# Performance work log

Measured on AMD Instinct MI355X. Metric: run time of the kernel, lower is better.

## Reference

```python
import jax, jax.numpy as jnp
import numpy as np

N = 30000      # nodes
E = 480000     # edges
H = 256        # hidden_dim (== input_dim)
T = 4          # n_etypes
G = 64         # graphs in batch
C = 10         # num_classes
STEPS = 5      # n_steps
EPS = 1e-5     # batchnorm eps


def setup_inputs() -> dict:
    key = jax.random.key(0)
    ks = jax.random.split(key, 20)
    s = 1.0 / np.sqrt(H)
    inp = {
        'feat': jax.random.normal(ks[0], (N, H), jnp.float32),
        'src': jax.random.randint(ks[1], (E,), 0, N, jnp.int32),
        'dst': jax.random.randint(ks[2], (E,), 0, N, jnp.int32),
        'etype': jax.random.randint(ks[3], (E,), 0, T, jnp.int32),
        'n2g': jnp.sort(jax.random.randint(ks[4], (N,), 0, G, jnp.int32)),
        # GatedGraphConv per-etype linears (shared across steps)
        'W_msg': jax.random.normal(ks[5], (T, H, H), jnp.float32) * s,
        'b_msg': jnp.zeros((T, H), jnp.float32),
        # GRUCell params (torch layout: [3H, H] for r,z,n)
        'w_ih': jax.random.normal(ks[6], (3 * H, H), jnp.float32) * s,
        'w_hh': jax.random.normal(ks[7], (3 * H, H), jnp.float32) * s,
        'b_ih': jnp.zeros((3 * H,), jnp.float32),
        'b_hh': jnp.zeros((3 * H,), jnp.float32),
        # BatchNorm1d affine params (training-mode batch stats)
        'bn_gamma': jnp.ones((H,), jnp.float32),
        'bn_beta': jnp.zeros((H,), jnp.float32),
        # GlobalAttentionPooling gate_nn = Linear(H, 1)
        'gate_w': jax.random.normal(ks[8], (H, 1), jnp.float32) * s,
        'gate_b': jnp.zeros((1,), jnp.float32),
        # classifier MLP
        'W1': jax.random.normal(ks[9], (H // 2, H), jnp.float32) * s,
        'b1': jnp.zeros((H // 2,), jnp.float32),
        'W2': jax.random.normal(ks[10], (C, H // 2), jnp.float32) * (1.0 / np.sqrt(H // 2)),
        'b2': jnp.zeros((C,), jnp.float32),
    }
    return inp


def reference(feat, src, dst, etype, n2g, W_msg, b_msg, w_ih, w_hh, b_ih, b_hh,
              bn_gamma, bn_beta, gate_w, gate_b, W1, b1, W2, b2):
    h = feat  # [N, H]; in_feats == out_feats so no zero-padding needed
    for _ in range(STEPS):
        # per-etype linear applied to all nodes, then gathered per edge (DGL semantics)
        Wh = jnp.einsum('nh,tkh->tnk', h, W_msg) + b_msg[:, None, :]  # [T, N, H]
        msgs = Wh[etype, src]                                         # [E, H]
        a = jax.ops.segment_sum(msgs, dst, num_segments=N)            # [N, H]
        # GRUCell(a, h)
        gi = a @ w_ih.T + b_ih
        gh = h @ w_hh.T + b_hh
        i_r, i_z, i_n = jnp.split(gi, 3, axis=-1)
        h_r, h_z, h_n = jnp.split(gh, 3, axis=-1)
        r = jax.nn.sigmoid(i_r + h_r)
        z = jax.nn.sigmoid(i_z + h_z)
        n = jnp.tanh(i_n + r * h_n)
        h = (1.0 - z) * n + z * h
    h2 = jax.nn.elu(h)
    # BatchNorm1d, training-mode batch statistics over all nodes
    mu = h2.mean(0)
    var = h2.var(0)
    h2 = (h2 - mu) * jax.lax.rsqrt(var + EPS) * bn_gamma + bn_beta
    # GlobalAttentionPooling: segment softmax over per-node gate scores
    gate = (h2 @ gate_w + gate_b)[:, 0]                               # [N]
    gmax = jax.ops.segment_max(gate, n2g, num_segments=G)
    e = jnp.exp(gate - gmax[n2g])
    denom = jax.ops.segment_sum(e, n2g, num_segments=G)
    alpha = (e / denom[n2g])[:, None]                                 # [N, 1]
    h_g = jax.ops.segment_sum(h2 * alpha, n2g, num_segments=G)        # [G, H]
    # classifier (dropout = identity in eval)
    x = jax.nn.relu(h_g @ W1.T + b1)
    return x @ W2.T + b2                                              # [G, C]
```

## Files before the change

kernel.cpp:

```cpp
#include <hip/hip_runtime.h>

#define NN 30000
#define EE 480000
#define HH 256
#define TT 4
#define GG 64
#define CC 10
#define MP 30080
#define SCAN_B 30
#define STB 120

typedef unsigned short u16;
typedef unsigned int u32;
typedef _Float16 f16;
typedef f16 half8 __attribute__((ext_vector_type(8)));
typedef f16 half4 __attribute__((ext_vector_type(4)));
typedef float f32x4 __attribute__((ext_vector_type(4)));

__device__ __forceinline__ u32 encf(float x) {
    u32 u = __float_as_uint(x);
    return (u & 0x80000000u) ? ~u : (u | 0x80000000u);
}
__device__ __forceinline__ float decf(u32 e) {
    u32 u = (e & 0x80000000u) ? (e ^ 0x80000000u) : ~e;
    return __uint_as_float(u);
}
__device__ __forceinline__ void gl_lds16(const void* g, void* l) {
    __builtin_amdgcn_global_load_lds(
        (const __attribute__((address_space(1))) void*)g,
        (__attribute__((address_space(3))) void*)l, 16, 0, 0);
}
__device__ __forceinline__ void xcd_map(int L, int& m0, int& col) {
    int idx = (L & 7) * 235 + (L >> 3);
    m0 = (idx >> 3) * 128;
    col = idx & 7;
}

__global__ void k_convert(const float* __restrict__ in, f16* __restrict__ o, int n) {
    int i = blockIdx.x * 256 + threadIdx.x;
    if (i < n) o[i] = (f16)in[i];
}

__global__ void k_pack_P(const float* __restrict__ w_ih, const float* __restrict__ w_hh,
                         f16* __restrict__ o) {
    int i = blockIdx.x * 256 + threadIdx.x;
    int p = i >> 9, k = i & 511;
    int g = p >> 7, t = p & 127;
    float v;
    if (t < 32) {
        int row = g * 32 + t;
        v = (k < 256) ? w_ih[row * 256 + k] : w_hh[row * 256 + (k - 256)];
    } else if (t < 64) {
        int row = 512 + g * 32 + (t - 32);
        v = (k < 256) ? w_ih[row * 256 + k] : 0.f;
    } else if (t < 96) {
        int row = 256 + g * 32 + (t - 64);
        v = (k < 256) ? w_ih[row * 256 + k] : w_hh[row * 256 + (k - 256)];
    } else {
        int row = 512 + g * 32 + (t - 96);
        v = (k >= 256) ? w_hh[row * 256 + (k - 256)] : 0.f;
    }
    o[i] = (f16)v;
}

__global__ void k_biasP(const float* __restrict__ b_ih, const float* __restrict__ b_hh,
                        float* __restrict__ bP) {
    int p = threadIdx.x + blockIdx.x * 256;
    if (p >= 1024) return;
    int g = p >> 7, t = p & 127;
    float v;
    if (t < 32)       { int r = g * 32 + t;            v = b_ih[r] + b_hh[r]; }
    else if (t < 64)  { int r = 512 + g * 32 + t - 32; v = b_ih[r]; }
    else if (t < 96)  { int r = 256 + g * 32 + t - 64; v = b_ih[r] + b_hh[r]; }
    else              { int r = 512 + g * 32 + t - 96; v = b_hh[r]; }
    bP[p] = v;
}

__global__ __launch_bounds__(256) void k_feat(const float* __restrict__ feat,
                                              f16* __restrict__ ah) {
    int n = blockIdx.x, c = threadIdx.x;
    float v = (n < NN) ? feat[(size_t)n * HH + c] : 0.f;
    ah[(size_t)n * 512 + 256 + c] = (f16)v;
}

__global__ void k_count(const int* __restrict__ dst, int* __restrict__ cnt) {
    int e = blockIdx.x * 256 + threadIdx.x;
    if (e < EE) atomicAdd(&cnt[dst[e]], 1);
}

__global__ __launch_bounds__(1024) void k_scan1(const int* __restrict__ cnt,
                                                int* __restrict__ rowptr,
                                                int* __restrict__ bsum) {
    __shared__ int buf[1024];
    int b = blockIdx.x, tid = threadIdx.x;
    int idx = b * 1024 + tid;
    int x = (idx < NN) ? cnt[idx] : 0;
    buf[tid] = x;
    __syncthreads();
    for (int ofs = 1; ofs < 1024; ofs <<= 1) {
        int v = (tid >= ofs) ? buf[tid - ofs] : 0;
        __syncthreads();
        buf[tid] += v;
        __syncthreads();
    }
    if (idx < NN) rowptr[idx] = buf[tid] - x;
    if (tid == 1023) bsum[b] = buf[1023];
}

__global__ void k_scan2(int* __restrict__ bsum) {
    __shared__ int s[SCAN_B];
    int tid = threadIdx.x;
    if (tid < SCAN_B) s[tid] = bsum[tid];
    __syncthreads();
    if (tid == 0) {
        int run = 0;
        for (int i = 0; i < SCAN_B; ++i) { int v = s[i]; s[i] = run; run += v; }
    }
    __syncthreads();
    if (tid < SCAN_B) bsum[tid] = s[tid];
}

__global__ __launch_bounds__(1024) void k_scan3(int* __restrict__ rowptr,
                                                const int* __restrict__ bsum,
                                                int* __restrict__ cur) {
    int b = blockIdx.x, tid = threadIdx.x;
    int idx = b * 1024 + tid;
    if (idx < NN) {
        int v = rowptr[idx] + bsum[b];
        rowptr[idx] = v;
        cur[idx] = v;
    }
    if (idx == 0) rowptr[NN] = EE;
}

__global__ void k_fill(const int* __restrict__ src, const int* __restrict__ dst,
                       const int* __restrict__ et, int* __restrict__ cur,
                       int* __restrict__ colpk) {
    int e = blockIdx.x * 256 + threadIdx.x;
    if (e < EE) {
        int pos = atomicAdd(&cur[dst[e]], 1);
        colpk[pos] = (et[e] << 16) | src[e];
    }
}

__global__ __launch_bounds__(256) void gemm_f16_o16(
    const f16* __restrict__ A, int lda,
    const f16* __restrict__ B, int ldb,
    const float* __restrict__ bias, f16* __restrict__ C, int ldc, int KT) {
    __shared__ f16 sA[8192], sB[8192];
    const int tid = threadIdx.x;
    const int lane = tid & 63;
    const int wv = tid >> 6;
    const int wr = wv >> 1, wc = wv & 1;
    int m0, colt;
    xcd_map(blockIdx.x, m0, colt);
    const int n0 = colt * 128;

    const int ldRow = tid >> 3;
    const int ldK = ((tid & 7) ^ (ldRow & 7)) * 8;
    const f16* aP = A + (size_t)(m0 + ldRow) * lda + ldK;
    const f16* bP = B + (size_t)(n0 + ldRow) * ldb + ldK;
    const size_t rstepA = (size_t)32 * lda;
    const size_t rstepB = (size_t)32 * ldb;

    const int wbyte = (tid & ~63) * 16;
    char* dA = (char*)sA + wbyte;
    char* dB = (char*)sB + wbyte;

    f32x4 acc[4][4];
#pragma unroll
    for (int i = 0; i < 4; i++)
#pragma unroll
        for (int j = 0; j < 4; j++) acc[i][j] = {0.f, 0.f, 0.f, 0.f};

    const int fr = lane & 15;
    const int l7 = lane & 7;
    const int cq = lane >> 4;
    const int p0 = (cq ^ l7) * 8;
    const int p1 = ((cq + 4) ^ l7) * 8;

    for (int kt = 0; kt < KT; ++kt) {
        const int k0 = kt * 64;
        __syncthreads();
        gl_lds16(aP + k0, dA);
        gl_lds16(aP + k0 + rstepA, dA + 4096);
        gl_lds16(aP + k0 + 2 * rstepA, dA + 8192);
        gl_lds16(aP + k0 + 3 * rstepA, dA + 12288);
        gl_lds16(bP + k0, dB);
        gl_lds16(bP + k0 + rstepB, dB + 4096);
        gl_lds16(bP + k0 + 2 * rstepB, dB + 8192);
        gl_lds16(bP + k0 + 3 * rstepB, dB + 12288);
        __syncthreads();

#pragma unroll
        for (int kk = 0; kk < 2; ++kk) {
            const int p = kk ? p1 : p0;
            half8 bh[4];
#pragma unroll
            for (int j = 0; j < 4; j++) {
                int brow = wc * 64 + j * 16 + fr;
                bh[j] = *(const half8*)&sB[brow * 64 + p];
            }
#pragma unroll
            for (int i = 0; i < 4; i++) {
                int arow = wr * 64 + i * 16 + fr;
                half8 ah = *(const half8*)&sA[arow * 64 + p];
#pragma unroll
                for (int j = 0; j < 4; j++)
                    acc[i][j] = __builtin_amdgcn_mfma_f32_16x16x32_f16(ah, bh[j], acc[i][j], 0, 0, 0);
            }
        }
    }

    const int lr = (lane >> 4) * 4;
    const int lc = lane & 15;
#pragma unroll
    for (int j = 0; j < 4; j++) {
        const int col = n0 + wc * 64 + j * 16 + lc;
        const float bj = bias[col];
#pragma unroll
        for (int i = 0; i < 4; i++) {
            const int rb = m0 + wr * 64 + i * 16 + lr;
#pragma unroll
            for (int r = 0; r < 4; r++)
                C[(size_t)(rb + r) * ldc + col] = (f16)(acc[i][j][r] + bj);
        }
    }
}

__global__ __launch_bounds__(256) void gemm_gruf(
    const f16* __restrict__ ahCur,
    const f16* __restrict__ wP,
    const float* __restrict__ bias,
    f16* __restrict__ ahNxt) {
    __shared__ f16 sA[8192], sB[8192];
    const int tid = threadIdx.x;
    const int lane = tid & 63;
    const int wv = tid >> 6;
    int m0, grp;
    xcd_map(blockIdx.x, m0, grp);
    const int n0 = grp * 128;
    const int gcol = grp * 32;

    const int ldRow = tid >> 3;
    const int ldK = ((tid & 7) ^ (ldRow & 7)) * 8;
    const f16* aP = ahCur + (size_t)(m0 + ldRow) * 512 + ldK;
    const f16* bPp = wP + (size_t)(n0 + ldRow) * 512 + ldK;
    const size_t rstep = (size_t)32 * 512;

    const int wbyte = (tid & ~63) * 16;
    char* dA = (char*)sA + wbyte;
    char* dB = (char*)sB + wbyte;

    f32x4 acc[2][8];
#pragma unroll
    for (int i = 0; i < 2; i++)
#pragma unroll
        for (int j = 0; j < 8; j++) acc[i][j] = {0.f, 0.f, 0.f, 0.f};

    const int fr = lane & 15;
    const int l7 = lane & 7;
    const int cq = lane >> 4;
    const int p0 = (cq ^ l7) * 8;
    const int p1 = ((cq + 4) ^ l7) * 8;

#pragma unroll
    for (int hf = 0; hf < 2; ++hf) {
        const int je = hf ? 6 : 2;
#pragma unroll 1
        for (int kt2 = 0; kt2 < 4; ++kt2) {
            const int k0 = (hf * 4 + kt2) * 64;
            __syncthreads();
            gl_lds16(aP + k0, dA);
            gl_lds16(aP + k0 + rstep, dA + 4096);
            gl_lds16(aP + k0 + 2 * rstep, dA + 8192);
            gl_lds16(aP + k0 + 3 * rstep, dA + 12288);
            gl_lds16(bPp + k0, dB);
            gl_lds16(bPp + k0 + rstep, dB + 4096);
            gl_lds16(bPp + k0 + 2 * rstep, dB + 8192);
            gl_lds16(bPp + k0 + 3 * rstep, dB + 12288);
            __syncthreads();

#pragma unroll
            for (int kk = 0; kk < 2; ++kk) {
                const int p = kk ? p1 : p0;
                const half8 a0 = *(const half8*)&sA[(wv * 32 + fr) * 64 + p];
                const half8 a1 = *(const half8*)&sA[(wv * 32 + 16 + fr) * 64 + p];
                half8 b;
                b = *(const half8*)&sB[(0 * 16 + fr) * 64 + p];
                acc[0][0] = __builtin_amdgcn_mfma_f32_16x16x32_f16(a0, b, acc[0][0], 0, 0, 0);
                acc[1][0] = __builtin_amdgcn_mfma_f32_16x16x32_f16(a1, b, acc[1][0], 0, 0, 0);
                b = *(const half8*)&sB[(1 * 16 + fr) * 64 + p];
                acc[0][1] = __builtin_amdgcn_mfma_f32_16x16x32_f16(a0, b, acc[0][1], 0, 0, 0);
                acc[1][1] = __builtin_amdgcn_mfma_f32_16x16x32_f16(a1, b, acc[1][1], 0, 0, 0);
                b = *(const half8*)&sB[(4 * 16 + fr) * 64 + p];
                acc[0][4] = __builtin_amdgcn_mfma_f32_16x16x32_f16(a0, b, acc[0][4], 0, 0, 0);
                acc[1][4] = __builtin_amdgcn_mfma_f32_16x16x32_f16(a1, b, acc[1][4], 0, 0, 0);
                b = *(const half8*)&sB[(5 * 16 + fr) * 64 + p];
                acc[0][5] = __builtin_amdgcn_mfma_f32_16x16x32_f16(a0, b, acc[0][5], 0, 0, 0);
                acc[1][5] = __builtin_amdgcn_mfma_f32_16x16x32_f16(a1, b, acc[1][5], 0, 0, 0);
                b = *(const half8*)&sB[(je * 16 + fr) * 64 + p];
                acc[0][je] = __builtin_amdgcn_mfma_f32_16x16x32_f16(a0, b, acc[0][je], 0, 0, 0);
                acc[1][je] = __builtin_amdgcn_mfma_f32_16x16x32_f16(a1, b, acc[1][je], 0, 0, 0);
                b = *(const half8*)&sB[((je + 1) * 16 + fr) * 64 + p];
                acc[0][je + 1] = __builtin_amdgcn_mfma_f32_16x16x32_f16(a0, b, acc[0][je + 1], 0, 0, 0);
                acc[1][je + 1] = __builtin_amdgcn_mfma_f32_16x16x32_f16(a1, b, acc[1][je + 1], 0, 0, 0);
            }
        }
    }

    const int lr = (lane >> 4) * 4;
    const int lc = lane & 15;
#pragma unroll
    for (int jj = 0; jj < 2; ++jj) {
        const int c32 = jj * 16 + lc;
        const float br = bias[n0 + c32];
        const float bi = bias[n0 + 32 + c32];
        const float bz = bias[n0 + 64 + c32];
        const float bn = bias[n0 + 96 + c32];
#pragma unroll
        for (int i = 0; i < 2; ++i) {
#pragma unroll
            for (int r = 0; r < 4; ++r) {
                const int n = m0 + wv * 32 + i * 16 + lr + r;
                float rv = acc[i][jj][r] + br;
                float iv = acc[i][jj + 2][r] + bi;
                float zv = acc[i][jj + 4][r] + bz;
                float nv = acc[i][jj + 6][r] + bn;
                float rr = 1.f / (1.f + expf(-rv));
                float zz = 1.f / (1.f + expf(-zv));
                float nn2 = tanhf(iv + rr * nv);
                size_t hidx = (size_t)n * 512 + 256 + gcol + c32;
                float hv = (float)ahCur[hidx];
                ahNxt[hidx] = (f16)((1.f - zz) * nn2 + zz * hv);
            }
        }
    }
}

__global__ __launch_bounds__(256) void k_agg(const f16* __restrict__ Wh,
                                             const int* __restrict__ rowptr,
                                             const int* __restrict__ colpk,
                                             f16* __restrict__ ah) {
    __shared__ int spk[256];
    __shared__ float4 sacc[3][64];
    const int n = blockIdx.x;
    const int tid = threadIdx.x;
    const int col4 = tid & 63;
    const int strip = tid >> 6;
    float4 acc = {0.f, 0.f, 0.f, 0.f};

    if (n < NN) {
        const int e0 = rowptr[n], e1 = rowptr[n + 1];
        for (int base = e0; base < e1; base += 256) {
            const int chunk = min(256, e1 - base);
            __syncthreads();
            if (tid < chunk) spk[tid] = colpk[base + tid];
            __syncthreads();
            int i = strip;
            for (; i + 4 < chunk; i += 8) {
                const int pk0 = spk[i], pk1 = spk[i + 4];
                const half4 v0 = *(const half4*)&Wh[(size_t)(pk0 & 0xFFFF) * 1024 + (pk0 >> 16) * 256 + col4 * 4];
                const half4 v1 = *(const half4*)&Wh[(size_t)(pk1 & 0xFFFF) * 1024 + (pk1 >> 16) * 256 + col4 * 4];
                acc.x += (float)v0.x + (float)v1.x;
                acc.y += (float)v0.y + (float)v1.y;
                acc.z += (float)v0.z + (float)v1.z;
                acc.w += (float)v0.w + (float)v1.w;
            }
            for (; i < chunk; i += 4) {
                const int pk = spk[i];
                const half4 v = *(const half4*)&Wh[(size_t)(pk & 0xFFFF) * 1024 + (pk >> 16) * 256 + col4 * 4];
                acc.x += (float)v.x;
                acc.y += (float)v.y;
                acc.z += (float)v.z;
                acc.w += (float)v.w;
            }
        }
    }
    if (strip) sacc[strip - 1][col4] = acc;
    __syncthreads();
    if (strip == 0 && n < NN) {
        const float4 t0 = sacc[0][col4], t1 = sacc[1][col4], t2 = sacc[2][col4];
        half4 o;
        o.x = (f16)(acc.x + t0.x + t1.x + t2.x);
        o.y = (f16)(acc.y + t0.y + t1.y + t2.y);
        o.z = (f16)(acc.z + t0.z + t1.z + t2.z);
        o.w = (f16)(acc.w + t0.w + t1.w + t2.w);
        *(half4*)&ah[(size_t)n * 512 + col4 * 4] = o;
    }
}

__global__ __launch_bounds__(256) void k_stats(const f16* __restrict__ ah,
                                               float* __restrict__ pbuf) {
    __shared__ float4 ssum[3][64], ssq[3][64];
    int tid = threadIdx.x, lane = tid & 63, w = tid >> 6;
    int c4 = lane * 4;
    float4 s = {0.f, 0.f, 0.f, 0.f}, q = {0.f, 0.f, 0.f, 0.f};
    for (int n = blockIdx.x * 4 + w; n < NN; n += STB * 4) {
        half4 v = *(const half4*)&ah[(size_t)n * 512 + 256 + c4];
        float ex = (float)v.x, ey = (float)v.y, ez = (float)v.z, ew = (float)v.w;
        ex = ex > 0.f ? ex : expm1f(ex);
        ey = ey > 0.f ? ey : expm1f(ey);
        ez = ez > 0.f ? ez : expm1f(ez);
        ew = ew > 0.f ? ew : expm1f(ew);
        s.x += ex; s.y += ey; s.z += ez; s.w += ew;
        q.x += ex * ex; q.y += ey * ey; q.z += ez * ez; q.w += ew * ew;
    }
    if (w) { ssum[w - 1][lane] = s; ssq[w - 1][lane] = q; }
    __syncthreads();
    if (w == 0) {
#pragma unroll
        for (int k = 0; k < 3; ++k) {
            float4 a = ssum[k][lane], b = ssq[k][lane];
            s.x += a.x; s.y += a.y; s.z += a.z; s.w += a.w;
            q.x += b.x; q.y += b.y; q.z += b.z; q.w += b.w;
        }
        *(float4*)&pbuf[blockIdx.x * 512 + c4] = s;
        *(float4*)&pbuf[blockIdx.x * 512 + 256 + c4] = q;
    }
}

__global__ __launch_bounds__(256) void k_prep(const float* __restrict__ pbuf,
                                              const float* __restrict__ gamma,
                                              const float* __restrict__ beta,
                                              const float* __restrict__ gate_w,
                                              const float* __restrict__ gate_b,
                                              float* __restrict__ wp,
                                              float* __restrict__ bnsum,
                                              float* __restrict__ bnsq) {
    __shared__ float red[256];
    int c = threadIdx.x;
    float s = 0.f, q = 0.f;
    for (int b = 0; b < STB; ++b) {
        s += pbuf[b * 512 + c];
        q += pbuf[b * 512 + 256 + c];
    }
    bnsum[c] = s;
    bnsq[c] = q;
    float mu = s * (1.f / NN);
    float var = q * (1.f / NN) - mu * mu;
    float rs = rsqrtf(var + 1e-5f);
    float gm = gamma[c], w = gate_w[c];
    wp[c] = rs * gm * w;
    red[c] = (beta[c] - mu * rs * gm) * w;
    __syncthreads();
    for (int st = 128; st > 0; st >>= 1) {
        if (c < st) red[c] += red[c + st];
        __syncthreads();
    }
    if (c == 0) wp[256] = red[0] + gate_b[0];
}

__global__ __launch_bounds__(256) void k_gate(const f16* __restrict__ ah,
                                              const float* __restrict__ wp,
                                              const int* __restrict__ n2g,
                                              float* __restrict__ gate,
                                              u32* __restrict__ gmaxenc) {
    __shared__ u32 smax[64];
    int tid = threadIdx.x;
    if (tid < 64) smax[tid] = 0;
    __syncthreads();
    int lane = tid & 63, wv = tid >> 6;
    int base = blockIdx.x * 128 + wv * 32;
    float4 w = ((const float4*)wp)[lane];
    float wc = wp[256];
    for (int k = 0; k < 32; ++k) {
        int n = base + k;
        if (n >= NN) break;
        half4 v = *(const half4*)&ah[(size_t)n * 512 + 256 + lane * 4];
        float ex = (float)v.x, ey = (float)v.y, ez = (float)v.z, ew = (float)v.w;
        ex = ex > 0.f ? ex : expm1f(ex);
        ey = ey > 0.f ? ey : expm1f(ey);
        ez = ez > 0.f ? ez : expm1f(ez);
        ew = ew > 0.f ? ew : expm1f(ew);
        float s = ex * w.x + ey * w.y + ez * w.z + ew * w.w;
#pragma unroll
        for (int off = 32; off; off >>= 1) s += __shfl_down(s, off);
        if (lane == 0) {
            float gt = s + wc;
            gate[n] = gt;
            atomicMax(&smax[n2g[n]], encf(gt));
        }
    }
    __syncthreads();
    if (tid < 64 && smax[tid]) atomicMax(&gmaxenc[tid], smax[tid]);
}

__global__ void k_expden(float* __restrict__ gate,
                         const int* __restrict__ n2g,
                         const u32* __restrict__ gmaxenc,
                         float* __restrict__ denom) {
    __shared__ float ssum[64];
    int tid = threadIdx.x;
    if (tid < 64) ssum[tid] = 0.f;
    __syncthreads();
    int n = blockIdx.x * 256 + tid;
    if (n < NN) {
        int g = n2g[n];
        float e = expf(gate[n] - decf(gmaxenc[g]));
        gate[n] = e;
        atomicAdd(&ssum[g], e);
    }
    __syncthreads();
    if (tid < 64 && ssum[tid] != 0.f) atomicAdd(&denom[tid], ssum[tid]);
}

__global__ __launch_bounds__(256) void k_pool(const f16* __restrict__ ah,
                                              const float* __restrict__ gate,
                                              const float* __restrict__ denom,
                                              const int* __restrict__ n2g,
                                              float* __restrict__ h_g) {
    int c = threadIdx.x;
    int r0 = blockIdx.x * 32, r1 = min(r0 + 32, NN);
    int gcur = -1;
    float accv = 0.f, inv = 0.f;
    for (int n = r0; n < r1; ++n) {
        int g = n2g[n];
        if (g != gcur) {
            if (gcur >= 0) atomicAdd(&h_g[gcur * HH + c], accv);
            gcur = g;
            accv = 0.f;
            inv = 1.f / denom[g];
        }
        float x = (float)ah[(size_t)n * 512 + 256 + c];
        x = x > 0.f ? x : expm1f(x);
        accv += gate[n] * inv * x;
    }
    if (gcur >= 0) atomicAdd(&h_g[gcur * HH + c], accv);
}

__global__ __launch_bounds__(256) void k_cls(const float* __restrict__ h_g,
                                             const float* __restrict__ bnsum,
                                             const float* __restrict__ bnsq,
                                             const float* __restrict__ gamma,
                                             const float* __restrict__ beta,
                                             const float* __restrict__ W1,
                                             const float* __restrict__ b1,
                                             const float* __restrict__ W2,
                                             const float* __restrict__ b2,
                                             float* __restrict__ out) {
    __shared__ float hg[256];
    __shared__ float x1[128];
    int g = blockIdx.x, tid = threadIdx.x;
    float mu = bnsum[tid] * (1.f / NN);
    float var = bnsq[tid] * (1.f / NN) - mu * mu;
    hg[tid] = (h_g[g * HH + tid] - mu) * rsqrtf(var + 1e-5f) * gamma[tid] + beta[tid];
    __syncthreads();
    if (tid < 128) {
        const float* w = W1 + tid * 256;
        float s = b1[tid];
#pragma unroll 8
        for (int c = 0; c < 256; ++c) s += hg[c] * w[c];
        x1[tid] = fmaxf(s, 0.f);
    }
    __syncthreads();
    if (tid < 10) {
        const float* w = W2 + tid * 128;
        float s = b2[tid];
        for (int j = 0; j < 128; ++j) s += x1[j] * w[j];
        out[g * CC + tid] = s;
    }
}

extern "C" void kernel_launch(void* const* d_in, const int* in_sizes, int n_in,
                              void* d_out, int out_size, void* d_ws, size_t ws_size,
                              hipStream_t stream) {
    const float* feat  = (const float*)d_in[0];
    const int*   src   = (const int*)d_in[1];
    const int*   dst   = (const int*)d_in[2];
    const int*   etype = (const int*)d_in[3];
    const int*   n2g   = (const int*)d_in[4];
    const float* W_msg = (const float*)d_in[5];
    const float* b_msg = (const float*)d_in[6];
    const float* w_ih  = (const float*)d_in[7];
    const float* w_hh  = (const float*)d_in[8];
    const float* b_ih  = (const float*)d_in[9];
    const float* b_hh  = (const float*)d_in[10];
    const float* bn_g  = (const float*)d_in[11];
    const float* bn_b  = (const float*)d_in[12];
    const float* gatew = (const float*)d_in[13];
    const float* gateb = (const float*)d_in[14];
    const float* W1    = (const float*)d_in[15];
    const float* b1    = (const float*)d_in[16];
    const float* W2    = (const float*)d_in[17];
    const float* b2    = (const float*)d_in[18];
    float* out = (float*)d_out;

    char* ws = (char*)d_ws;
    size_t off = 0;
    auto alloc = [&](size_t bytes) -> char* {
        char* p = ws + off;
        off += (bytes + 255) & ~(size_t)255;
        return p;
    };

    const size_t ZZ = (size_t)(NN + 64 + 64 + GG * HH) * 4;
    char* zz = alloc(ZZ);
    int*   cnt     = (int*)zz;
    float* denom   = (float*)(zz + (size_t)NN * 4);
    u32*   gmaxenc = (u32*)(denom + 64);
    float* h_g     = (float*)(gmaxenc + 64);

    int* rowptr = (int*)alloc((NN + 1) * 4);
    int* cur    = (int*)alloc(NN * 4);
    int* bsum   = (int*)alloc(SCAN_B * 4);
    int* colpk  = (int*)alloc((size_t)EE * 4);
    float* gate = (float*)alloc(NN * 4);
    float* wp   = (float*)alloc(260 * 4);
    float* bP   = (float*)alloc(1024 * 4);
    float* pbuf = (float*)alloc((size_t)STB * 512 * 4);
    float* bnsum = (float*)alloc(256 * 4);
    float* bnsq  = (float*)alloc(256 * 4);

    f16* ahb[2];
    ahb[0] = (f16*)alloc((size_t)MP * 512 * 2);
    ahb[1] = (f16*)alloc((size_t)MP * 512 * 2);

    f16* wmsg = (f16*)alloc((size_t)1024 * 256 * 2);
    f16* wP   = (f16*)alloc((size_t)1024 * 512 * 2);
    f16* Wh   = (f16*)alloc((size_t)MP * 1024 * 2);

    hipMemsetAsync(zz, 0, ZZ, stream);

    k_convert<<<1024, 256, 0, stream>>>(W_msg, wmsg, 1024 * 256);
    k_pack_P<<<2048, 256, 0, stream>>>(w_ih, w_hh, wP);
    k_biasP<<<4, 256, 0, stream>>>(b_ih, b_hh, bP);
    k_feat<<<MP, 256, 0, stream>>>(feat, ahb[0]);

    k_count<<<(EE + 255) / 256, 256, 0, stream>>>(dst, cnt);
    k_scan1<<<SCAN_B, 1024, 0, stream>>>(cnt, rowptr, bsum);
    k_scan2<<<1, 64, 0, stream>>>(bsum);
    k_scan3<<<SCAN_B, 1024, 0, stream>>>(rowptr, bsum, cur);
    k_fill<<<(EE + 255) / 256, 256, 0, stream>>>(src, dst, etype, cur, colpk);

    for (int s = 0; s < 5; ++s) {
        f16* ahC = ahb[s & 1];
        f16* ahN = ahb[1 - (s & 1)];
        gemm_f16_o16<<<1880, 256, 0, stream>>>(
            ahC + 256, 512, wmsg, 256, b_msg, Wh, 1024, 4);
        k_agg<<<MP, 256, 0, stream>>>(Wh, rowptr, colpk, ahC);
        gemm_gruf<<<1880, 256, 0, stream>>>(ahC, wP, bP, ahN);
    }
    f16* ahF = ahb[1];

    k_stats<<<STB, 256, 0, stream>>>(ahF, pbuf);
    k_prep<<<1, 256, 0, stream>>>(pbuf, bn_g, bn_b, gatew, gateb, wp, bnsum, bnsq);
    k_gate<<<235, 256, 0, stream>>>(ahF, wp, n2g, gate, gmaxenc);
    k_expden<<<(NN + 255) / 256, 256, 0, stream>>>(gate, n2g, gmaxenc, denom);
    k_pool<<<MP / 32, 256, 0, stream>>>(ahF, gate, denom, n2g, h_g);
    k_cls<<<GG, 256, 0, stream>>>(h_g, bnsum, bnsq, bn_g, bn_b, W1, b1, W2, b2, out);

    (void)in_sizes; (void)n_in; (void)out_size; (void)ws_size;
}
```

Baseline: 847.7 us.

## Aggregate raw hidden states per etype before applying message linear

Reorders the message step: each destination node first sums neighbour hidden states into four per-etype buckets (plus edge-type counts for the bias), then one GEMM with K=1088 multiplies by the concatenated W_msg and bias. This replaces the N×1024 Wh GEMM output and its gather with a gather over the 256-wide h rows, cutting the intermediate write and read traffic. The price is a larger GEMM K per node (1088 vs 256), four accumulator sets with branching in the gather, and fp16 rounding of the summed features and counts.

```diff
diff --git a/kernel.cpp b/kernel.cpp
--- a/kernel.cpp
+++ b/kernel.cpp
@@ -9,6 +9,7 @@
 #define MP 30080
 #define SCAN_B 30
 #define STB 120
+#define KU 1088
 
 typedef unsigned short u16;
 typedef unsigned int u32;
@@ -36,9 +37,16 @@
     col = idx & 7;
 }
 
-__global__ void k_convert(const float* __restrict__ in, f16* __restrict__ o, int n) {
+__global__ void k_pack_W(const float* __restrict__ W_msg, const float* __restrict__ b_msg,
+                         f16* __restrict__ o) {
     int i = blockIdx.x * 256 + threadIdx.x;
-    if (i < n) o[i] = (f16)in[i];
+    if (i >= 256 * KU) return;
+    int k = i / KU, j = i % KU;
+    float v;
+    if (j < 1024) { int t = j >> 8, hh = j & 255; v = W_msg[((t << 8) + k) * 256 + hh]; }
+    else if (j < 1028) v = b_msg[(j - 1024) * 256 + k];
+    else v = 0.f;
+    o[i] = (f16)v;
 }
 
 __global__ void k_pack_P(const float* __restrict__ w_ih, const float* __restrict__ w_hh,
@@ -143,25 +151,101 @@
     }
 }
 
-__global__ __launch_bounds__(256) void gemm_f16_o16(
-    const f16* __restrict__ A, int lda,
-    const f16* __restrict__ B, int ldb,
-    const float* __restrict__ bias, f16* __restrict__ C, int ldc, int KT) {
+__global__ __launch_bounds__(256) void k_aggh(const f16* __restrict__ ah,
+                                              const int* __restrict__ rowptr,
+                                              const int* __restrict__ colpk,
+                                              f16* __restrict__ u) {
+    __shared__ int spk[256];
+    __shared__ float4 sacc[3][4][64];
+    __shared__ int scnt[4][4];
+    const int n = blockIdx.x;
+    const int tid = threadIdx.x;
+    const int col4 = tid & 63;
+    const int strip = tid >> 6;
+    float4 a0 = {0,0,0,0}, a1 = {0,0,0,0}, a2 = {0,0,0,0}, a3 = {0,0,0,0};
+    int c0 = 0, c1 = 0, c2 = 0, c3 = 0;
+
+    if (n < NN) {
+        const int e0 = rowptr[n], e1 = rowptr[n + 1];
+        for (int base = e0; base < e1; base += 256) {
+            const int chunk = min(256, e1 - base);
+            __syncthreads();
+            if (tid < chunk) spk[tid] = colpk[base + tid];
+            __syncthreads();
+            for (int i = strip; i < chunk; i += 4) {
+                const int pk = spk[i];
+                const half4 v = *(const half4*)&ah[(size_t)(pk & 0xFFFF) * 512 + 256 + col4 * 4];
+                const int t = pk >> 16;
+                if (t == 0)      { a0.x += (float)v.x; a0.y += (float)v.y; a0.z += (float)v.z; a0.w += (float)v.w; c0++; }
+                else if (t == 1) { a1.x += (float)v.x; a1.y += (float)v.y; a1.z += (float)v.z; a1.w += (float)v.w; c1++; }
+                else if (t == 2) { a2.x += (float)v.x; a2.y += (float)v.y; a2.z += (float)v.z; a2.w += (float)v.w; c2++; }
+                else             { a3.x += (float)v.x; a3.y += (float)v.y; a3.z += (float)v.z; a3.w += (float)v.w; c3++; }
+            }
+        }
+    }
+    if (strip) {
+        sacc[strip - 1][0][col4] = a0;
+        sacc[strip - 1][1][col4] = a1;
+        sacc[strip - 1][2][col4] = a2;
+        sacc[strip - 1][3][col4] = a3;
+        if (col4 == 0) { scnt[strip][0] = c0; scnt[strip][1] = c1; scnt[strip][2] = c2; scnt[strip][3] = c3; }
+    } else if (col4 == 0) {
+        scnt[0][0] = c0; scnt[0][1] = c1; scnt[0][2] = c2; scnt[0][3] = c3;
+    }
+    __syncthreads();
+    if (strip == 0 && n < NN) {
+#pragma unroll
+        for (int s2 = 0; s2 < 3; ++s2) {
+            float4 t;
+            t = sacc[s2][0][col4]; a0.x += t.x; a0.y += t.y; a0.z += t.z; a0.w += t.w;
+            t = sacc[s2][1][col4]; a1.x += t.x; a1.y += t.y; a1.z += t.z; a1.w += t.w;
+            t = sacc[s2][2][col4]; a2.x += t.x; a2.y += t.y; a2.z += t.z; a2.w += t.w;
+            t = sacc[s2][3][col4]; a3.x += t.x; a3.y += t.y; a3.z += t.z; a3.w += t.w;
+        }
+        f16* ur = u + (size_t)n * KU;
+        half4 o;
+        o.x = (f16)a0.x; o.y = (f16)a0.y; o.z = (f16)a0.z; o.w = (f16)a0.w;
+        *(half4*)&ur[0 * 256 + col4 * 4] = o;
+        o.x = (f16)a1.x; o.y = (f16)a1.y; o.z = (f16)a1.z; o.w = (f16)a1.w;
+        *(half4*)&ur[1 * 256 + col4 * 4] = o;
+        o.x = (f16)a2.x; o.y = (f16)a2.y; o.z = (f16)a2.z; o.w = (f16)a2.w;
+        *(half4*)&ur[2 * 256 + col4 * 4] = o;
+        o.x = (f16)a3.x; o.y = (f16)a3.y; o.z = (f16)a3.z; o.w = (f16)a3.w;
+        *(half4*)&ur[3 * 256 + col4 * 4] = o;
+        if (col4 < 16) {
+            float vals[4];
+#pragma unroll
+            for (int r = 0; r < 4; ++r) {
+                int c = col4 * 4 + r;
+                vals[r] = (c < 4) ? (float)(scnt[0][c] + scnt[1][c] + scnt[2][c] + scnt[3][c]) : 0.f;
+            }
+            half4 cv;
+            cv.x = (f16)vals[0]; cv.y = (f16)vals[1]; cv.z = (f16)vals[2]; cv.w = (f16)vals[3];
+            *(half4*)&ur[1024 + col4 * 4] = cv;
+        }
+    }
+}
+
+__global__ __launch_bounds__(256) void gemm_a(
+    const f16* __restrict__ A,
+    const f16* __restrict__ B,
+    f16* __restrict__ C) {
     __shared__ f16 sA[8192], sB[8192];
     const int tid = threadIdx.x;
     const int lane = tid & 63;
     const int wv = tid >> 6;
     const int wr = wv >> 1, wc = wv & 1;
-    int m0, colt;
-    xcd_map(blockIdx.x, m0, colt);
-    const int n0 = colt * 128;
+    const int idx = (blockIdx.x & 7) * 59 + (blockIdx.x >> 3);
+    const int m0 = (idx >> 1) * 128;
+    if (m0 >= MP) return;
+    const int n0 = (idx & 1) * 128;
 
     const int ldRow = tid >> 3;
     const int ldK = ((tid & 7) ^ (ldRow & 7)) * 8;
-    const f16* aP = A + (size_t)(m0 + ldRow) * lda + ldK;
-    const f16* bP = B + (size_t)(n0 + ldRow) * ldb + ldK;
-    const size_t rstepA = (size_t)32 * lda;
-    const size_t rstepB = (size_t)32 * ldb;
+    const f16* aP = A + (size_t)(m0 + ldRow) * KU + ldK;
+    const f16* bP = B + (size_t)(n0 + ldRow) * KU + ldK;
+    const size_t rstepA = (size_t)32 * KU;
+    const size_t rstepB = (size_t)32 * KU;
 
     const int wbyte = (tid & ~63) * 16;
     char* dA = (char*)sA + wbyte;
@@ -179,7 +263,7 @@
     const int p0 = (cq ^ l7) * 8;
     const int p1 = ((cq + 4) ^ l7) * 8;
 
-    for (int kt = 0; kt < KT; ++kt) {
+    for (int kt = 0; kt < 17; ++kt) {
         const int k0 = kt * 64;
         __syncthreads();
         gl_lds16(aP + k0, dA);
@@ -204,10 +288,10 @@
 #pragma unroll
             for (int i = 0; i < 4; i++) {
                 int arow = wr * 64 + i * 16 + fr;
-                half8 ah = *(const half8*)&sA[arow * 64 + p];
+                half8 av = *(const half8*)&sA[arow * 64 + p];
 #pragma unroll
                 for (int j = 0; j < 4; j++)
-                    acc[i][j] = __builtin_amdgcn_mfma_f32_16x16x32_f16(ah, bh[j], acc[i][j], 0, 0, 0);
+                    acc[i][j] = __builtin_amdgcn_mfma_f32_16x16x32_f16(av, bh[j], acc[i][j], 0, 0, 0);
             }
         }
     }
@@ -217,13 +301,12 @@
 #pragma unroll
     for (int j = 0; j < 4; j++) {
         const int col = n0 + wc * 64 + j * 16 + lc;
-        const float bj = bias[col];
 #pragma unroll
         for (int i = 0; i < 4; i++) {
             const int rb = m0 + wr * 64 + i * 16 + lr;
 #pragma unroll
             for (int r = 0; r < 4; r++)
-                C[(size_t)(rb + r) * ldc + col] = (f16)(acc[i][j][r] + bj);
+                C[(size_t)(rb + r) * 512 + col] = (f16)acc[i][j][r];
         }
     }
 }
@@ -338,58 +421,6 @@
     }
 }
 
-__global__ __launch_bounds__(256) void k_agg(const f16* __restrict__ Wh,
-                                             const int* __restrict__ rowptr,
-                                             const int* __restrict__ colpk,
-                                             f16* __restrict__ ah) {
-    __shared__ int spk[256];
-    __shared__ float4 sacc[3][64];
-    const int n = blockIdx.x;
-    const int tid = threadIdx.x;
-    const int col4 = tid & 63;
-    const int strip = tid >> 6;
-    float4 acc = {0.f, 0.f, 0.f, 0.f};
-
-    if (n < NN) {
-        const int e0 = rowptr[n], e1 = rowptr[n + 1];
-        for (int base = e0; base < e1; base += 256) {
-            const int chunk = min(256, e1 - base);
-            __syncthreads();
-            if (tid < chunk) spk[tid] = colpk[base + tid];
-            __syncthreads();
-            int i = strip;
-            for (; i + 4 < chunk; i += 8) {
-                const int pk0 = spk[i], pk1 = spk[i + 4];
-                const half4 v0 = *(const half4*)&Wh[(size_t)(pk0 & 0xFFFF) * 1024 + (pk0 >> 16) * 256 + col4 * 4];
-                const half4 v1 = *(const half4*)&Wh[(size_t)(pk1 & 0xFFFF) * 1024 + (pk1 >> 16) * 256 + col4 * 4];
-                acc.x += (float)v0.x + (float)v1.x;
-                acc.y += (float)v0.y + (float)v1.y;
-                acc.z += (float)v0.z + (float)v1.z;
-                acc.w += (float)v0.w + (float)v1.w;
-            }
-            for (; i < chunk; i += 4) {
-                const int pk = spk[i];
-                const half4 v = *(const half4*)&Wh[(size_t)(pk & 0xFFFF) * 1024 + (pk >> 16) * 256 + col4 * 4];
-                acc.x += (float)v.x;
-                acc.y += (float)v.y;
-                acc.z += (float)v.z;
-                acc.w += (float)v.w;
-            }
-        }
-    }
-    if (strip) sacc[strip - 1][col4] = acc;
-    __syncthreads();
-    if (strip == 0 && n < NN) {
-        const float4 t0 = sacc[0][col4], t1 = sacc[1][col4], t2 = sacc[2][col4];
-        half4 o;
-        o.x = (f16)(acc.x + t0.x + t1.x + t2.x);
-        o.y = (f16)(acc.y + t0.y + t1.y + t2.y);
-        o.z = (f16)(acc.z + t0.z + t1.z + t2.z);
-        o.w = (f16)(acc.w + t0.w + t1.w + t2.w);
-        *(half4*)&ah[(size_t)n * 512 + col4 * 4] = o;
-    }
-}
-
 __global__ __launch_bounds__(256) void k_stats(const f16* __restrict__ ah,
                                                float* __restrict__ pbuf) {
     __shared__ float4 ssum[3][64], ssq[3][64];
@@ -616,13 +647,13 @@
     ahb[0] = (f16*)alloc((size_t)MP * 512 * 2);
     ahb[1] = (f16*)alloc((size_t)MP * 512 * 2);
 
-    f16* wmsg = (f16*)alloc((size_t)1024 * 256 * 2);
+    f16* Wcat = (f16*)alloc((size_t)256 * KU * 2);
     f16* wP   = (f16*)alloc((size_t)1024 * 512 * 2);
-    f16* Wh   = (f16*)alloc((size_t)MP * 1024 * 2);
+    f16* u    = (f16*)alloc((size_t)MP * KU * 2);
 
     hipMemsetAsync(zz, 0, ZZ, stream);
 
-    k_convert<<<1024, 256, 0, stream>>>(W_msg, wmsg, 1024 * 256);
+    k_pack_W<<<(256 * KU + 255) / 256, 256, 0, stream>>>(W_msg, b_msg, Wcat);
     k_pack_P<<<2048, 256, 0, stream>>>(w_ih, w_hh, wP);
     k_biasP<<<4, 256, 0, stream>>>(b_ih, b_hh, bP);
     k_feat<<<MP, 256, 0, stream>>>(feat, ahb[0]);
@@ -636,9 +667,8 @@
     for (int s = 0; s < 5; ++s) {
         f16* ahC = ahb[s & 1];
         f16* ahN = ahb[1 - (s & 1)];
-        gemm_f16_o16<<<1880, 256, 0, stream>>>(
-            ahC + 256, 512, wmsg, 256, b_msg, Wh, 1024, 4);
-        k_agg<<<MP, 256, 0, stream>>>(Wh, rowptr, colpk, ahC);
+        k_aggh<<<MP, 256, 0, stream>>>(ahC, rowptr, colpk, u);
+        gemm_a<<<472, 256, 0, stream>>>(u, Wcat, ahC);
         gemm_gruf<<<1880, 256, 0, stream>>>(ahC, wP, bP, ahN);
     }
     f16* ahF = ahb[1];
```

Result: slower. 949.9 us (+12.1%).
